# Kernel tuning notes

Measured on AMD Instinct MI355X. Metric: run time of the kernel, lower is better.

## Reference

```python
import jax, jax.numpy as jnp
import numpy as np

N = 100000
IN_CH = 256
HID = 256
HEADS = 1
LAYERS = 2
ALPHA = 0.5
EPS = 1e-5


def _layernorm(x, g, b):
    mu = x.mean(axis=-1, keepdims=True)
    var = ((x - mu) ** 2).mean(axis=-1, keepdims=True)
    return (x - mu) * jax.lax.rsqrt(var + EPS) * g + b


def setup_inputs() -> dict:
    key = jax.random.key(0)
    ks = jax.random.split(key, 12)
    s_in = 1.0 / np.sqrt(IN_CH)
    s_h = 1.0 / np.sqrt(HID)
    return {
        "x": jax.random.normal(ks[0], (N, IN_CH), dtype=jnp.float32),
        "fc_w": jax.random.uniform(ks[1], (HID, IN_CH), minval=-s_in, maxval=s_in, dtype=jnp.float32),
        "fc_b": jax.random.uniform(ks[2], (HID,), minval=-s_in, maxval=s_in, dtype=jnp.float32),
        "Wq_w": jax.random.uniform(ks[3], (LAYERS, HEADS * HID, HID), minval=-s_h, maxval=s_h, dtype=jnp.float32),
        "Wq_b": jax.random.uniform(ks[4], (LAYERS, HEADS * HID), minval=-s_h, maxval=s_h, dtype=jnp.float32),
        "Wk_w": jax.random.uniform(ks[5], (LAYERS, HEADS * HID, HID), minval=-s_h, maxval=s_h, dtype=jnp.float32),
        "Wk_b": jax.random.uniform(ks[6], (LAYERS, HEADS * HID), minval=-s_h, maxval=s_h, dtype=jnp.float32),
        "Wv_w": jax.random.uniform(ks[7], (LAYERS, HEADS * HID, HID), minval=-s_h, maxval=s_h, dtype=jnp.float32),
        "Wv_b": jax.random.uniform(ks[8], (LAYERS, HEADS * HID), minval=-s_h, maxval=s_h, dtype=jnp.float32),
        "ln_g": jnp.ones((LAYERS + 1, HID), dtype=jnp.float32),
        "ln_b": jnp.zeros((LAYERS + 1, HID), dtype=jnp.float32),
    }


def _linear_attention(q, k, v):
    # q:[N,H,M] k:[L,H,M] v:[L,H,D]; global-Frobenius-norm normalization as in torch.norm(x, p=2)
    n = q.shape[0]
    q = q / jnp.linalg.norm(q)
    k = k / jnp.linalg.norm(k)
    kvs = jnp.einsum('lhm,lhd->hmd', k, v)            # tiny [H,M,D]
    num = jnp.einsum('nhm,hmd->nhd', q, kvs) + n * v  # [N,H,D]
    ks_sum = k.sum(axis=0)                            # [H,M]
    denom = jnp.einsum('nhm,hm->nh', q, ks_sum)[..., None] + n
    return num / denom


def reference(x, fc_w, fc_b, Wq_w, Wq_b, Wk_w, Wk_b, Wv_w, Wv_b, ln_g, ln_b):
    h = jax.nn.relu(_layernorm(x @ fc_w.T + fc_b, ln_g[0], ln_b[0]))
    prev = h
    for i in range(LAYERS):
        q = (h @ Wq_w[i].T + Wq_b[i]).reshape(-1, HEADS, HID)
        k = (h @ Wk_w[i].T + Wk_b[i]).reshape(-1, HEADS, HID)
        v = (h @ Wv_w[i].T + Wv_b[i]).reshape(-1, HEADS, HID)
        attn = _linear_attention(q, k, v).mean(axis=1)  # [N,HID]
        h = ALPHA * attn + (1.0 - ALPHA) * prev
        h = jax.nn.relu(_layernorm(h, ln_g[i + 1], ln_b[i + 1]))
        prev = h
    return h
```

## Files before the change

### kernel.cpp

```cpp
#include <hip/hip_runtime.h>

#define NV 100000
#define NVf 100000.0f
#define NPAD 100032LL
#define CHUNKS 1563
#define NBG 48

typedef __attribute__((ext_vector_type(8))) short bf16x8;
typedef __attribute__((ext_vector_type(4))) float f32x4;

constexpr size_t SB      = (size_t)NPAD * 256 * 2;
constexpr size_t OFF_XB  = 0;
constexpr size_t OFF_H0  = SB;
constexpr size_t OFF_WB  = 2 * SB;
constexpr size_t OFF_GBF = OFF_WB + (size_t)7 * 65536 * 2;
constexpr size_t OFF_PQ  = OFF_GBF + 131072;
constexpr size_t OFF_PK  = OFF_PQ + 131072;
constexpr size_t OFF_KVT = OFF_PK + 131072;
constexpr size_t OFF_WEF = OFF_KVT + 131072;
constexpr size_t OFF_HP  = OFF_WEF + 131072;
constexpr size_t OFF_KSH = OFF_HP + 131072;
constexpr size_t OFF_VSH = OFF_KSH + 1024;
constexpr size_t OFF_U   = OFF_VSH + 1024;
constexpr size_t OFF_BE  = OFF_U + 1024;
constexpr size_t OFF_RED = OFF_BE + 1024;

__device__ __forceinline__ float b2f(unsigned h) {
  unsigned u = h << 16;
  return __builtin_bit_cast(float, u);
}
__device__ __forceinline__ unsigned short f2bf(float x) {
  unsigned u = __builtin_bit_cast(unsigned, x);
  u = (u + 0x7fffu + ((u >> 16) & 1u)) >> 16;
  return (unsigned short)u;
}
__device__ __forceinline__ void async16(void* lds, const void* g) {
  __builtin_amdgcn_global_load_lds((const __attribute__((address_space(1))) unsigned*)g,
                                   (__attribute__((address_space(3))) unsigned*)lds,
                                   16, 0, 0);
}
template <int GRAN>
__device__ __forceinline__ bf16x8 frag_strided(const uint4* t, int nbase, int col) {
  const unsigned short* sp = (const unsigned short*)t;
  bf16x8 f;
  int ch = col >> 3, cl = col & 7;
#pragma unroll
  for (int i = 0; i < 8; ++i) {
    int n = nbase + i;
    f[i] = (short)sp[(n * GRAN + ((ch ^ n) & (GRAN - 1))) * 8 + cl];
  }
  return f;
}

__global__ void k_zero(char* ws) {
  int i = blockIdx.x * 256 + threadIdx.x;
  *(float4*)((float*)(ws + OFF_HP) + (size_t)i * 4) = make_float4(0.f, 0.f, 0.f, 0.f);
}

__global__ void k_conv(const float* __restrict__ x, const float* __restrict__ fcw,
                       const float* __restrict__ wq, const float* __restrict__ wk,
                       const float* __restrict__ wv, char* __restrict__ ws) {
  long long t = (long long)blockIdx.x * 256 + threadIdx.x;
  if (t < 6400000LL) {
    float4 v = ((const float4*)x)[t];
    unsigned lo = (unsigned)f2bf(v.x) | ((unsigned)f2bf(v.y) << 16);
    unsigned hi = (unsigned)f2bf(v.z) | ((unsigned)f2bf(v.w) << 16);
    ((uint2*)(ws + OFF_XB))[t] = make_uint2(lo, hi);
  } else {
    long long u = t - 6400000LL;
    if (u < 114688LL) {
      int e4 = (int)(u << 2);
      int slot = e4 >> 16, within = e4 & 65535;
      const float* src;
      if (slot == 0) src = fcw + within;
      else {
        int s = slot - 1, l = s / 3, k = s % 3;
        src = (k == 0 ? wq : (k == 1 ? wk : wv)) + l * 65536 + within;
      }
      float4 v = *(const float4*)src;
      unsigned lo = (unsigned)f2bf(v.x) | ((unsigned)f2bf(v.y) << 16);
      unsigned hi = (unsigned)f2bf(v.z) | ((unsigned)f2bf(v.w) << 16);
      ((uint2*)(ws + OFF_WB))[u] = make_uint2(lo, hi);
    }
  }
}

__global__ __launch_bounds__(256) void outpass(
    const unsigned short* __restrict__ A,
    const unsigned short* __restrict__ W,
    const float* __restrict__ bias,
    const float* __restrict__ lng, const float* __restrict__ lnb,
    const float* __restrict__ u, const float* __restrict__ beff,
    const float* __restrict__ red,
    float* __restrict__ hpart,
    unsigned short* __restrict__ outB, float* __restrict__ outF, int mode) {
  __shared__ uint4 sH4[2048];
  __shared__ uint4 sW4[2048];
  __shared__ float sMisc[704];

  const int tid = threadIdx.x;
  const int w = tid >> 6, lane = tid & 63, quad = lane >> 4, lc = lane & 15;
  const int c0 = w * 64;
  const long long n0 = (long long)blockIdx.x * 64;

#pragma unroll
  for (int it = 0; it < 8; ++it) {
    int s = it * 256 + tid;
    int n = s >> 5, gl = s & 31, g = gl ^ (n & 31);
    async16(&sH4[s], A + (size_t)(n0 + n) * 256 + g * 8);
  }

  f32x4 acc[4][4];
  for (int i = 0; i < 4; ++i)
    for (int j = 0; j < 4; ++j) acc[i][j] = (f32x4){0.f, 0.f, 0.f, 0.f};

  for (int kc = 0; kc < 4; ++kc) {
#pragma unroll
    for (int it = 0; it < 8; ++it) {
      int s = it * 256 + tid;
      int j = s >> 3, gl = s & 7, g = gl ^ (j & 7);
      async16(&sW4[s], W + (size_t)j * 256 + kc * 64 + g * 8);
    }
    __syncthreads();
#pragma unroll
    for (int kk = 0; kk < 2; ++kk) {
      bf16x8 af[4], bv[4];
      for (int fr = 0; fr < 4; ++fr) {
        int m = fr * 16 + lc;
        af[fr] = __builtin_bit_cast(bf16x8, sH4[m * 32 + (((kc * 8 + kk * 4 + quad) ^ m) & 31)]);
      }
      for (int fc = 0; fc < 4; ++fc) {
        int j = c0 + fc * 16 + lc;
        bv[fc] = __builtin_bit_cast(bf16x8, sW4[j * 8 + (((kk * 4 + quad) ^ j) & 7)]);
      }
      for (int fr = 0; fr < 4; ++fr)
        for (int fc = 0; fc < 4; ++fc)
          acc[fr][fc] = __builtin_amdgcn_mfma_f32_16x16x32_bf16(af[fr], bv[fc], acc[fr][fc], 0, 0, 0);
    }
    __syncthreads();
  }

  const bool attn = (mode != 0);
  if (attn) {
    int row = tid >> 2, p = tid & 3;
    float rd = 0.f;
    const float4* u4 = (const float4*)u;
#pragma unroll
    for (int g8 = 0; g8 < 8; ++g8) {
      int g = p * 8 + g8;
      uint4 hv = sH4[row * 32 + ((g ^ row) & 31)];
      float4 ua = u4[g * 2], ub = u4[g * 2 + 1];
      rd += b2f(hv.x & 0xffffu) * ua.x + b2f(hv.x >> 16) * ua.y
          + b2f(hv.y & 0xffffu) * ua.z + b2f(hv.y >> 16) * ua.w
          + b2f(hv.z & 0xffffu) * ub.x + b2f(hv.z >> 16) * ub.y
          + b2f(hv.w & 0xffffu) * ub.z + b2f(hv.w >> 16) * ub.w;
    }
    sMisc[tid] = rd;
  }
  __syncthreads();
  if (attn && tid < 64) {
    float s = sMisc[tid * 4] + sMisc[tid * 4 + 1] + sMisc[tid * 4 + 2] + sMisc[tid * 4 + 3];
    sMisc[640 + tid] = 1.0f / (s + red[2]);
  }
  __syncthreads();

  float gv[4], bb[4], be[4], bq[4];
  for (int fc = 0; fc < 4; ++fc) {
    int j = c0 + fc * 16 + lc;
    gv[fc] = lng[j]; bb[fc] = lnb[j];
    if (attn) be[fc] = beff[j]; else bq[fc] = bias[j];
  }

  for (int fr = 0; fr < 4; ++fr) {
    int rrb = fr * 16 + quad * 4;
    float s1[4] = {0, 0, 0, 0}, s2[4] = {0, 0, 0, 0};
    for (int fc = 0; fc < 4; ++fc) {
      int j = c0 + fc * 16 + lc;
      for (int r = 0; r < 4; ++r) {
        int m = rrb + r;
        float v = acc[fr][fc][r];
        if (attn) {
          float hm = b2f(((const unsigned short*)sH4)[(m * 32 + (((j >> 3) ^ m) & 31)) * 8 + (j & 7)]);
          v = 0.5f * ((v + be[fc]) * sMisc[640 + m]) + 0.5f * hm;
        } else v += bq[fc];
        acc[fr][fc][r] = v;
        s1[r] += v; s2[r] += v * v;
      }
    }
    for (int r = 0; r < 4; ++r) {
      float a = s1[r], b = s2[r];
      a += __shfl_xor(a, 1); b += __shfl_xor(b, 1);
      a += __shfl_xor(a, 2); b += __shfl_xor(b, 2);
      a += __shfl_xor(a, 4); b += __shfl_xor(b, 4);
      a += __shfl_xor(a, 8); b += __shfl_xor(b, 8);
      if (lc == 0) { sMisc[w * 64 + rrb + r] = a; sMisc[256 + w * 64 + rrb + r] = b; }
    }
  }
  __syncthreads();
  if (tid < 64) {
    float S = sMisc[tid] + sMisc[64 + tid] + sMisc[128 + tid] + sMisc[192 + tid];
    float Q = sMisc[256 + tid] + sMisc[320 + tid] + sMisc[384 + tid] + sMisc[448 + tid];
    float mean = S * (1.f / 256.f);
    float var = Q * (1.f / 256.f) - mean * mean;
    sMisc[512 + tid] = mean; sMisc[576 + tid] = rsqrtf(var + 1e-5f);
  }
  __syncthreads();

  if (mode < 2) {
    float cs[4] = {0, 0, 0, 0};
    unsigned short* sT = (unsigned short*)sW4;
    for (int fr = 0; fr < 4; ++fr)
      for (int fc = 0; fc < 4; ++fc) {
        int j = c0 + fc * 16 + lc;
        for (int r = 0; r < 4; ++r) {
          int m = fr * 16 + quad * 4 + r;
          float y = (acc[fr][fc][r] - sMisc[512 + m]) * sMisc[576 + m] * gv[fc] + bb[fc];
          y = fmaxf(y, 0.f);
          if (n0 + m >= NV) y = 0.f;
          cs[fc] += y;
          sT[(m * 32 + (((j >> 3) ^ m) & 31)) * 8 + (j & 7)] = f2bf(y);
        }
      }
    __syncthreads();
    {
      int row = tid >> 2;
      uint4* dst = (uint4*)(outB + (size_t)(n0 + row) * 256);
#pragma unroll
      for (int i = 0; i < 8; ++i) {
        int g = i * 4 + (tid & 3);
        dst[g] = sW4[row * 32 + ((g ^ row) & 31)];
      }
    }
    for (int fc = 0; fc < 4; ++fc) {
      float c = cs[fc];
      c += __shfl_xor(c, 16); c += __shfl_xor(c, 32);
      if (quad == 0) atomicAdd(&hpart[(blockIdx.x & 63) * 256 + c0 + fc * 16 + lc], c);
    }
  } else {
    float* sTf = (float*)sW4;
    for (int hh = 0; hh < 2; ++hh) {
      if (hh) __syncthreads();
      for (int fr = hh * 2; fr < hh * 2 + 2; ++fr)
        for (int fc = 0; fc < 4; ++fc) {
          int j = c0 + fc * 16 + lc;
          for (int r = 0; r < 4; ++r) {
            int m = fr * 16 + quad * 4 + r, r32 = m - hh * 32;
            float y = (acc[fr][fc][r] - sMisc[512 + m]) * sMisc[576 + m] * gv[fc] + bb[fc];
            y = fmaxf(y, 0.f);
            sTf[(r32 * 64 + (((j >> 2) ^ r32) & 63)) * 4 + (j & 3)] = y;
          }
        }
      __syncthreads();
      int row32 = tid >> 3;
      long long n = n0 + hh * 32 + row32;
      if (n < NV) {
        uint4* dst = (uint4*)(outF + n * 256);
#pragma unroll
        for (int i = 0; i < 8; ++i) {
          int g = i * 8 + (tid & 7);
          dst[g] = sW4[row32 * 64 + ((g ^ row32) & 63)];
        }
      }
    }
  }
}

__global__ __launch_bounds__(256) void gpass(const unsigned short* __restrict__ H,
                                             float* __restrict__ gpart) {
  __shared__ uint4 sHa4[1024], sHb4[1024];
  const int tid = threadIdx.x;
  const int w = tid >> 6, lane = tid & 63, quad = lane >> 4, lc = lane & 15;
  const int qm = blockIdx.y & 1, qj = blockIdx.y >> 1;
  const int mw = (w & 1) * 64, jw = (w >> 1) * 64;

  f32x4 acc[4][4];
  for (int i = 0; i < 4; ++i)
    for (int j = 0; j < 4; ++j) acc[i][j] = (f32x4){0.f, 0.f, 0.f, 0.f};

  for (int c = blockIdx.x; c < CHUNKS; c += NBG) {
#pragma unroll
    for (int it = 0; it < 4; ++it) {
      int s = it * 256 + tid;
      int n = s >> 4, gl = s & 15, g = gl ^ (n & 15);
      const unsigned short* rowp = H + ((size_t)c * 64 + n) * 256;
      async16(&sHa4[s], rowp + qm * 128 + g * 8);
      async16(&sHb4[s], rowp + qj * 128 + g * 8);
    }
    __syncthreads();
#pragma unroll
    for (int kk = 0; kk < 2; ++kk) {
      bf16x8 af[4], bv[4];
      for (int fr = 0; fr < 4; ++fr)
        af[fr] = frag_strided<16>(sHa4, kk * 32 + quad * 8, mw + fr * 16 + lc);
      for (int jf = 0; jf < 4; ++jf)
        bv[jf] = frag_strided<16>(sHb4, kk * 32 + quad * 8, jw + jf * 16 + lc);
      for (int fr = 0; fr < 4; ++fr)
        for (int jf = 0; jf < 4; ++jf)
          acc[fr][jf] = __builtin_amdgcn_mfma_f32_16x16x32_bf16(af[fr], bv[jf], acc[fr][jf], 0, 0, 0);
    }
    __syncthreads();
  }
  float* gp = gpart + (size_t)blockIdx.x * 65536;
  for (int fr = 0; fr < 4; ++fr)
    for (int jf = 0; jf < 4; ++jf) {
      int row = qm * 128 + mw + fr * 16 + quad * 4;
      int col = qj * 128 + jw + jf * 16 + lc;
      for (int r = 0; r < 4; ++r)
        gp[(size_t)(row + r) * 256 + col] = acc[fr][jf][r];
    }
}

__global__ __launch_bounds__(256) void s0ker(
    const float* __restrict__ gpart, const float* __restrict__ hpart,
    const unsigned short* __restrict__ wq, const unsigned short* __restrict__ wk,
    const unsigned short* __restrict__ wv,
    const float* __restrict__ bq, const float* __restrict__ bk,
    unsigned short* __restrict__ Gbf, float* __restrict__ ksh0, float* __restrict__ vsh0,
    float* __restrict__ red) {
  const int tid = threadIdx.x;
  if (blockIdx.x < 64) {
    size_t idx = ((size_t)blockIdx.x * 256 + tid) * 4;
    float a = 0, b = 0, c = 0, d = 0;
    for (int p = 0; p < NBG; ++p) {
      float4 v = *(const float4*)(gpart + (size_t)p * 65536 + idx);
      a += v.x; b += v.y; c += v.z; d += v.w;
    }
    unsigned lo = (unsigned)f2bf(a) | ((unsigned)f2bf(b) << 16);
    unsigned hi = (unsigned)f2bf(c) | ((unsigned)f2bf(d) << 16);
    *(uint2*)(Gbf + idx) = make_uint2(lo, hi);
    return;
  }
  __shared__ float sH[256], sA[256], sBv[256];
  float hs = 0;
  for (int r = 0; r < 64; ++r) hs += hpart[r * 256 + tid];
  sH[tid] = hs;
  __syncthreads();
  float sk = 0, sv = 0, sq = 0;
  for (int g = 0; g < 32; ++g) {
    uint4 wk4 = *(const uint4*)(wk + (size_t)tid * 256 + g * 8);
    uint4 wv4 = *(const uint4*)(wv + (size_t)tid * 256 + g * 8);
    uint4 wq4 = *(const uint4*)(wq + (size_t)tid * 256 + g * 8);
    unsigned uk[4] = {wk4.x, wk4.y, wk4.z, wk4.w};
    unsigned uv[4] = {wv4.x, wv4.y, wv4.z, wv4.w};
    unsigned uq[4] = {wq4.x, wq4.y, wq4.z, wq4.w};
    for (int h = 0; h < 4; ++h) {
      float h0 = sH[g * 8 + h * 2], h1 = sH[g * 8 + h * 2 + 1];
      sk += b2f(uk[h] & 0xffffu) * h0 + b2f(uk[h] >> 16) * h1;
      sv += b2f(uv[h] & 0xffffu) * h0 + b2f(uv[h] >> 16) * h1;
      sq += b2f(uq[h] & 0xffffu) * h0 + b2f(uq[h] >> 16) * h1;
    }
  }
  ksh0[tid] = sk; vsh0[tid] = sv;
  sA[tid]  = 2.f * bq[tid] * sq + NVf * bq[tid] * bq[tid];
  sBv[tid] = 2.f * bk[tid] * sk + NVf * bk[tid] * bk[tid];
  __syncthreads();
  if (tid == 0) {
    float a = 0, b = 0;
    for (int i = 0; i < 256; ++i) { a += sA[i]; b += sBv[i]; }
    red[0] = a; red[1] = b;
  }
}

__global__ __launch_bounds__(256) void ks12(
    const unsigned short* __restrict__ A0, const unsigned short* __restrict__ A1,
    const unsigned short* __restrict__ B,
    unsigned short* __restrict__ O0, unsigned short* __restrict__ O1,
    const float* __restrict__ ksh0, const float* __restrict__ vsh0,
    const float* __restrict__ bk, const float* __restrict__ bv,
    float* __restrict__ red, int mode) {
  __shared__ uint4 sA4[512], sB4[2048];
  __shared__ float sRd[4];
  const int tid = threadIdx.x;
  const int w = tid >> 6, lane = tid & 63, quad = lane >> 4, lc = lane & 15;
  const int c0 = w * 64;
  const int mat = (mode == 2) ? 0 : (blockIdx.x >> 2);
  const int mt  = (mode == 2) ? blockIdx.x : (blockIdx.x & 3);
  const unsigned short* A = mat ? A1 : A0;
  unsigned short* O = mat ? O1 : O0;

  f32x4 acc[4][4];
  for (int i = 0; i < 4; ++i)
    for (int j = 0; j < 4; ++j) acc[i][j] = (f32x4){0.f, 0.f, 0.f, 0.f};

  for (int kc = 0; kc < 4; ++kc) {
#pragma unroll
    for (int it = 0; it < 2; ++it) {
      int s = it * 256 + tid;
      int m = s >> 3, gl = s & 7, g = gl ^ (m & 7);
      async16(&sA4[s], A + (size_t)(mt * 64 + m) * 256 + kc * 64 + g * 8);
    }
#pragma unroll
    for (int it = 0; it < 8; ++it) {
      int s = it * 256 + tid;
      int j = s >> 3, gl = s & 7, g = gl ^ (j & 7);
      async16(&sB4[s], B + (size_t)j * 256 + kc * 64 + g * 8);
    }
    __syncthreads();
#pragma unroll
    for (int kk = 0; kk < 2; ++kk) {
      bf16x8 af[4], bv4[4];
      for (int fr = 0; fr < 4; ++fr) {
        int m = fr * 16 + lc;
        af[fr] = __builtin_bit_cast(bf16x8, sA4[m * 8 + (((kk * 4 + quad) ^ m) & 7)]);
      }
      for (int fc = 0; fc < 4; ++fc) {
        int j = c0 + fc * 16 + lc;
        bv4[fc] = __builtin_bit_cast(bf16x8, sB4[j * 8 + (((kk * 4 + quad) ^ j) & 7)]);
      }
      for (int fr = 0; fr < 4; ++fr)
        for (int fc = 0; fc < 4; ++fc)
          acc[fr][fc] = __builtin_amdgcn_mfma_f32_16x16x32_bf16(af[fr], bv4[fc], acc[fr][fc], 0, 0, 0);
    }
    __syncthreads();
  }

  unsigned short* sT = (unsigned short*)sB4;
  if (mode != 2) {
    float tr = 0.f;
    for (int fr = 0; fr < 4; ++fr)
      for (int fc = 0; fc < 4; ++fc) {
        int j = c0 + fc * 16 + lc;
        for (int r = 0; r < 4; ++r) {
          int mL = fr * 16 + quad * 4 + r;
          float v = acc[fr][fc][r];
          tr += v * b2f(A[(size_t)(mt * 64 + mL) * 256 + j]);
          sT[(mL * 32 + (((j >> 3) ^ mL) & 31)) * 8 + (j & 7)] = f2bf(v);
        }
      }
    for (int msk = 1; msk <= 32; msk <<= 1) tr += __shfl_xor(tr, msk);
    if (lane == 0) sRd[w] = tr;
    __syncthreads();
    int row = tid >> 2;
    uint4* dst = (uint4*)(O + (size_t)(mt * 64 + row) * 256);
#pragma unroll
    for (int i = 0; i < 8; ++i) {
      int g = i * 4 + (tid & 3);
      dst[g] = sB4[row * 32 + ((g ^ row) & 31)];
    }
    if (tid == 0) atomicAdd(&red[mat], sRd[0] + sRd[1] + sRd[2] + sRd[3]);
  } else {
    for (int fr = 0; fr < 4; ++fr)
      for (int fc = 0; fc < 4; ++fc) {
        int d = c0 + fc * 16 + lc;
        for (int r = 0; r < 4; ++r) {
          int mL = fr * 16 + quad * 4 + r, mrow = mt * 64 + mL;
          float v = acc[fr][fc][r] + ksh0[mrow] * bv[d] + bk[mrow] * (vsh0[d] + NVf * bv[d]);
          sT[(d * 8 + (((mL >> 3) ^ d) & 7)) * 8 + (mL & 7)] = f2bf(v);
        }
      }
    __syncthreads();
    for (int p = 0; p < 4; ++p) {
      int d = p * 64 + (tid >> 2);
#pragma unroll
      for (int i = 0; i < 2; ++i) {
        int g = i * 4 + (tid & 3);
        *(uint4*)(O0 + (size_t)d * 256 + mt * 64 + g * 8) = sB4[d * 8 + ((g ^ d) & 7)];
      }
    }
  }
}

__global__ __launch_bounds__(256) void ks3(
    const unsigned short* __restrict__ KVT, const unsigned short* __restrict__ wq,
    const unsigned short* __restrict__ wv,
    const float* __restrict__ ksh0,
    const float* __restrict__ bq, const float* __restrict__ bk, const float* __restrict__ bv,
    unsigned short* __restrict__ Wef, float* __restrict__ uvec, float* __restrict__ bev,
    float* __restrict__ red) {
  const int tid = threadIdx.x;
  if (blockIdx.x == 4) {
    __shared__ float sV[256], sC[256];
    float gam = rsqrtf(red[0]) * rsqrtf(red[1]);
    sV[tid] = ksh0[tid] + NVf * bk[tid];
    __syncthreads();
    float s = 0;
    for (int m = 0; m < 256; ++m) s += b2f(wq[(size_t)m * 256 + tid]) * sV[m];
    uvec[tid] = gam * s;
    float s2 = 0;
    const uint4* kr = (const uint4*)(KVT + (size_t)tid * 256);
    for (int g = 0; g < 32; ++g) {
      uint4 v = kr[g];
      unsigned uu[4] = {v.x, v.y, v.z, v.w};
      for (int h = 0; h < 4; ++h) {
        s2 += b2f(uu[h] & 0xffffu) * bq[g * 8 + h * 2] + b2f(uu[h] >> 16) * bq[g * 8 + h * 2 + 1];
      }
    }
    bev[tid] = gam * s2 + NVf * bv[tid];
    sC[tid] = bq[tid] * sV[tid];
    __syncthreads();
    if (tid == 0) {
      float t = 0;
      for (int i = 0; i < 256; ++i) t += sC[i];
      red[2] = gam * t + NVf;
    }
    return;
  }
  __shared__ uint4 sA4[2048], sB4[2048];
  const int w = tid >> 6, lane = tid & 63, quad = lane >> 4, lc = lane & 15;
  const int c0 = w * 64, dt = blockIdx.x;
#pragma unroll
  for (int it = 0; it < 8; ++it) {
    int s = it * 256 + tid;
    int n = s >> 5, gl = s & 31, g = gl ^ (n & 31);
    async16(&sA4[s], KVT + (size_t)(dt * 64 + n) * 256 + g * 8);
  }
  f32x4 acc[4][4];
  for (int i = 0; i < 4; ++i)
    for (int j = 0; j < 4; ++j) acc[i][j] = (f32x4){0.f, 0.f, 0.f, 0.f};
  for (int kc = 0; kc < 4; ++kc) {
#pragma unroll
    for (int it = 0; it < 8; ++it) {
      int s = it * 256 + tid;
      int n = s >> 5, gl = s & 31, g = gl ^ (n & 31);
      async16(&sB4[s], wq + (size_t)(kc * 64 + n) * 256 + g * 8);
    }
    __syncthreads();
#pragma unroll
    for (int kk = 0; kk < 2; ++kk) {
      bf16x8 af[4], bv4[4];
      for (int fr = 0; fr < 4; ++fr) {
        int dL = fr * 16 + lc;
        af[fr] = __builtin_bit_cast(bf16x8, sA4[dL * 32 + (((kc * 8 + kk * 4 + quad) ^ dL) & 31)]);
      }
      for (int fc = 0; fc < 4; ++fc)
        bv4[fc] = frag_strided<32>(sB4, kk * 32 + quad * 8, c0 + fc * 16 + lc);
      for (int fr = 0; fr < 4; ++fr)
        for (int fc = 0; fc < 4; ++fc)
          acc[fr][fc] = __builtin_amdgcn_mfma_f32_16x16x32_bf16(af[fr], bv4[fc], acc[fr][fc], 0, 0, 0);
    }
    __syncthreads();
  }
  float gam = rsqrtf(red[0]) * rsqrtf(red[1]);
  unsigned short* sT = (unsigned short*)sB4;
  for (int fr = 0; fr < 4; ++fr)
    for (int fc = 0; fc < 4; ++fc) {
      int a = c0 + fc * 16 + lc;
      for (int r = 0; r < 4; ++r) {
        int dL = fr * 16 + quad * 4 + r;
        float v = gam * acc[fr][fc][r] + NVf * b2f(wv[(size_t)(dt * 64 + dL) * 256 + a]);
        sT[(dL * 32 + (((a >> 3) ^ dL) & 31)) * 8 + (a & 7)] = f2bf(v);
      }
    }
  __syncthreads();
  int row = tid >> 2;
  uint4* dst = (uint4*)(Wef + (size_t)(dt * 64 + row) * 256);
#pragma unroll
  for (int i = 0; i < 8; ++i) {
    int g = i * 4 + (tid & 3);
    dst[g] = sB4[row * 32 + ((g ^ row) & 31)];
  }
}

extern "C" void kernel_launch(void* const* d_in, const int* in_sizes, int n_in,
                              void* d_out, int out_size, void* d_ws, size_t ws_size,
                              hipStream_t stream) {
  const float* x   = (const float*)d_in[0];
  const float* fcw = (const float*)d_in[1];
  const float* fcb = (const float*)d_in[2];
  const float* wqw = (const float*)d_in[3];
  const float* wqb = (const float*)d_in[4];
  const float* wkw = (const float*)d_in[5];
  const float* wkb = (const float*)d_in[6];
  const float* wvw = (const float*)d_in[7];
  const float* wvb = (const float*)d_in[8];
  const float* lng = (const float*)d_in[9];
  const float* lnb = (const float*)d_in[10];
  char* ws = (char*)d_ws;
  float* out = (float*)d_out;

  unsigned short* xb  = (unsigned short*)(ws + OFF_XB);
  unsigned short* h0  = (unsigned short*)(ws + OFF_H0);
  unsigned short* h1  = xb;
  unsigned short* wb  = (unsigned short*)(ws + OFF_WB);
  unsigned short* Gbf = (unsigned short*)(ws + OFF_GBF);
  unsigned short* Pq  = (unsigned short*)(ws + OFF_PQ);
  unsigned short* Pk  = (unsigned short*)(ws + OFF_PK);
  unsigned short* KVT = (unsigned short*)(ws + OFF_KVT);
  unsigned short* Wef = (unsigned short*)(ws + OFF_WEF);
  float* hp   = (float*)(ws + OFF_HP);
  float* kshv = (float*)(ws + OFF_KSH);
  float* vshv = (float*)(ws + OFF_VSH);
  float* uvec = (float*)(ws + OFF_U);
  float* bev  = (float*)(ws + OFF_BE);
  float* red  = (float*)(ws + OFF_RED);
  float* gpart = out;

  k_zero<<<32, 256, 0, stream>>>(ws);
  k_conv<<<25448, 256, 0, stream>>>(x, fcw, wqw, wkw, wvw, ws);

  outpass<<<1563, 256, 0, stream>>>(xb, wb, fcb, lng, lnb,
                                    nullptr, nullptr, nullptr, hp, h0, nullptr, 0);

  for (int l = 0; l < 2; ++l) {
    const unsigned short* wq = wb + (size_t)(1 + 3 * l) * 65536;
    const unsigned short* wk = wq + 65536;
    const unsigned short* wv = wk + 65536;
    const float* bq = wqb + l * 256;
    const float* bk = wkb + l * 256;
    const float* bv = wvb + l * 256;
    unsigned short* hin = l ? h1 : h0;
    float* hpIn = hp + (size_t)l * 16384;

    gpass<<<dim3(NBG, 4), 256, 0, stream>>>(hin, gpart);
    s0ker<<<65, 256, 0, stream>>>(gpart, hpIn, wq, wk, wv, bq, bk, Gbf, kshv, vshv, red);
    ks12<<<8, 256, 0, stream>>>(wq, wk, Gbf, Pq, Pk, nullptr, nullptr, nullptr, nullptr, red, 0);
    ks12<<<4, 256, 0, stream>>>(Pk, nullptr, wv, KVT, nullptr, kshv, vshv, bk, bv, red, 2);
    ks3<<<5, 256, 0, stream>>>(KVT, wq, wv, kshv, bq, bk, bv, Wef, uvec, bev, red);

    outpass<<<1563, 256, 0, stream>>>(hin, Wef, nullptr,
                                      lng + (size_t)(l + 1) * 256, lnb + (size_t)(l + 1) * 256,
                                      uvec, bev, red,
                                      (l == 0) ? (hp + 16384) : nullptr,
                                      (l == 0) ? h1 : nullptr,
                                      (l == 1) ? out : nullptr, l + 1);
  }
}
```

Before: 747.4 us.

## Stream weights from global in outpass, enlarge gpass chunks and grid

The outpass GEMM no longer stages weight tiles through shared memory. Each lane loads its bf16 weight fragments straight from global/L2, which removes the shared W buffer and the per-k-chunk barriers, and the fp32 output is written directly without a shared-memory transpose. Occupancy hints of 3 blocks per CU are added. The gram pass now processes 96-row chunks with 128 blocks instead of 64-row chunks with 48 blocks, aiming for more parallelism and fewer loop iterations. The trade-off is uncoalesced global reads of the weights and scattered fp32 stores, plus more partial Gram matrices to reduce unless later code changes.

```diff
diff --git a/kernel.cpp b/kernel.cpp
--- a/kernel.cpp
+++ b/kernel.cpp
@@ -3,8 +3,8 @@
 #define NV 100000
 #define NVf 100000.0f
 #define NPAD 100032LL
-#define CHUNKS 1563
-#define NBG 48
+#define CH96 1042
+#define NBG 128
 
 typedef __attribute__((ext_vector_type(8))) short bf16x8;
 typedef __attribute__((ext_vector_type(4))) float f32x4;
@@ -85,7 +85,7 @@
   }
 }
 
-__global__ __launch_bounds__(256) void outpass(
+__global__ __launch_bounds__(256, 3) void outpass(
     const unsigned short* __restrict__ A,
     const unsigned short* __restrict__ W,
     const float* __restrict__ bias,
@@ -95,7 +95,6 @@
     float* __restrict__ hpart,
     unsigned short* __restrict__ outB, float* __restrict__ outF, int mode) {
   __shared__ uint4 sH4[2048];
-  __shared__ uint4 sW4[2048];
   __shared__ float sMisc[704];
 
   const int tid = threadIdx.x;
@@ -109,35 +108,29 @@
     int n = s >> 5, gl = s & 31, g = gl ^ (n & 31);
     async16(&sH4[s], A + (size_t)(n0 + n) * 256 + g * 8);
   }
+  __syncthreads();
 
   f32x4 acc[4][4];
   for (int i = 0; i < 4; ++i)
     for (int j = 0; j < 4; ++j) acc[i][j] = (f32x4){0.f, 0.f, 0.f, 0.f};
 
-  for (int kc = 0; kc < 4; ++kc) {
-#pragma unroll
-    for (int it = 0; it < 8; ++it) {
-      int s = it * 256 + tid;
-      int j = s >> 3, gl = s & 7, g = gl ^ (j & 7);
-      async16(&sW4[s], W + (size_t)j * 256 + kc * 64 + g * 8);
-    }
-    __syncthreads();
-#pragma unroll
-    for (int kk = 0; kk < 2; ++kk) {
-      bf16x8 af[4], bv[4];
-      for (int fr = 0; fr < 4; ++fr) {
-        int m = fr * 16 + lc;
-        af[fr] = __builtin_bit_cast(bf16x8, sH4[m * 32 + (((kc * 8 + kk * 4 + quad) ^ m) & 31)]);
-      }
-      for (int fc = 0; fc < 4; ++fc) {
-        int j = c0 + fc * 16 + lc;
-        bv[fc] = __builtin_bit_cast(bf16x8, sW4[j * 8 + (((kk * 4 + quad) ^ j) & 7)]);
-      }
-      for (int fr = 0; fr < 4; ++fr)
-        for (int fc = 0; fc < 4; ++fc)
-          acc[fr][fc] = __builtin_amdgcn_mfma_f32_16x16x32_bf16(af[fr], bv[fc], acc[fr][fc], 0, 0, 0);
-    }
-    __syncthreads();
+  const unsigned short* wp[4];
+#pragma unroll
+  for (int fc = 0; fc < 4; ++fc)
+    wp[fc] = W + (size_t)(c0 + fc * 16 + lc) * 256 + quad * 8;
+
+#pragma unroll
+  for (int kq = 0; kq < 8; ++kq) {
+    bf16x8 bv[4], af[4];
+    for (int fc = 0; fc < 4; ++fc)
+      bv[fc] = *(const bf16x8*)(wp[fc] + kq * 32);
+    for (int fr = 0; fr < 4; ++fr) {
+      int m = fr * 16 + lc;
+      af[fr] = __builtin_bit_cast(bf16x8, sH4[m * 32 + ((kq * 4 + quad) ^ (m & 31))]);
+    }
+    for (int fr = 0; fr < 4; ++fr)
+      for (int fc = 0; fc < 4; ++fc)
+        acc[fr][fc] = __builtin_amdgcn_mfma_f32_16x16x32_bf16(af[fr], bv[fc], acc[fr][fc], 0, 0, 0);
   }
 
   const bool attn = (mode != 0);
@@ -208,7 +201,7 @@
 
   if (mode < 2) {
     float cs[4] = {0, 0, 0, 0};
-    unsigned short* sT = (unsigned short*)sW4;
+    unsigned short* sT = (unsigned short*)sH4;
     for (int fr = 0; fr < 4; ++fr)
       for (int fc = 0; fc < 4; ++fc) {
         int j = c0 + fc * 16 + lc;
@@ -228,7 +221,7 @@
 #pragma unroll
       for (int i = 0; i < 8; ++i) {
         int g = i * 4 + (tid & 3);
-        dst[g] = sW4[row * 32 + ((g ^ row) & 31)];
+        dst[g] = sH4[row * 32 + ((g ^ row) & 31)];
       }
     }
     for (int fc = 0; fc < 4; ++fc) {
@@ -237,37 +230,23 @@
       if (quad == 0) atomicAdd(&hpart[(blockIdx.x & 63) * 256 + c0 + fc * 16 + lc], c);
     }
   } else {
-    float* sTf = (float*)sW4;
-    for (int hh = 0; hh < 2; ++hh) {
-      if (hh) __syncthreads();
-      for (int fr = hh * 2; fr < hh * 2 + 2; ++fr)
-        for (int fc = 0; fc < 4; ++fc) {
-          int j = c0 + fc * 16 + lc;
-          for (int r = 0; r < 4; ++r) {
-            int m = fr * 16 + quad * 4 + r, r32 = m - hh * 32;
-            float y = (acc[fr][fc][r] - sMisc[512 + m]) * sMisc[576 + m] * gv[fc] + bb[fc];
-            y = fmaxf(y, 0.f);
-            sTf[(r32 * 64 + (((j >> 2) ^ r32) & 63)) * 4 + (j & 3)] = y;
-          }
+    for (int fr = 0; fr < 4; ++fr)
+      for (int fc = 0; fc < 4; ++fc) {
+        int j = c0 + fc * 16 + lc;
+        for (int r = 0; r < 4; ++r) {
+          int m = fr * 16 + quad * 4 + r;
+          long long n = n0 + m;
+          float y = (acc[fr][fc][r] - sMisc[512 + m]) * sMisc[576 + m] * gv[fc] + bb[fc];
+          y = fmaxf(y, 0.f);
+          if (n < NV) outF[(size_t)n * 256 + j] = y;
         }
-      __syncthreads();
-      int row32 = tid >> 3;
-      long long n = n0 + hh * 32 + row32;
-      if (n < NV) {
-        uint4* dst = (uint4*)(outF + n * 256);
-#pragma unroll
-        for (int i = 0; i < 8; ++i) {
-          int g = i * 8 + (tid & 7);
-          dst[g] = sW4[row32 * 64 + ((g ^ row32) & 63)];
-        }
-      }
-    }
-  }
-}
-
-__global__ __launch_bounds__(256) void gpass(const unsigned short* __restrict__ H,
-                                             float* __restrict__ gpart) {
-  __shared__ uint4 sHa4[1024], sHb4[1024];
+      }
+  }
+}
+
+__global__ __launch_bounds__(256, 3) void gpass(const unsigned short* __restrict__ H,
+                                                float* __restrict__ gpart) {
+  __shared__ uint4 sHa4[1536], sHb4[1536];
   const int tid = threadIdx.x;
   const int w = tid >> 6, lane = tid & 63, quad = lane >> 4, lc = lane & 15;
   const int qm = blockIdx.y & 1, qj = blockIdx.y >> 1;
@@ -277,18 +256,18 @@
   for (int i = 0; i < 4; ++i)
     for (int j = 0; j < 4; ++j) acc[i][j] = (f32x4){0.f, 0.f, 0.f, 0.f};
 
-  for (int c = blockIdx.x; c < CHUNKS; c += NBG) {
-#pragma unroll
-    for (int it = 0; it < 4; ++it) {
+  for (int c = blockIdx.x; c < CH96; c += NBG) {
+#pragma unroll
+    for (int it = 0; it < 6; ++it) {
       int s = it * 256 + tid;
       int n = s >> 4, gl = s & 15, g = gl ^ (n & 15);
-      const unsigned short* rowp = H + ((size_t)c * 64 + n) * 256;
+      const unsigned short* rowp = H + ((size_t)c * 96 + n) * 256;
       async16(&sHa4[s], rowp + qm * 128 + g * 8);
       async16(&sHb4[s], rowp + qj * 128 + g * 8);
     }
     __syncthreads();
 #pragma unroll
-    for (int kk = 0; kk < 2; ++kk) {
+    for (int kk = 0; kk < 3; ++kk) {
       bf16x8 af[4], bv[4];
       for (int fr = 0; fr < 4; ++fr)
         af[fr] = frag_strided<16>(sHa4, kk * 32 + quad * 8, mw + fr * 16 + lc);
```

After: 904.6 us. +21.0%, slower.
